# Optimization experiments

Hardware: AMD Instinct MI355X
Metric: run time of the kernel (lower is better)

## Reference

```python
import jax, jax.numpy as jnp
import numpy as np
import math

N, I, H, O = 2048, 16, 64, 64
CUTS, HEADS_DIM, GROUPS = 8, 8, 4
RADIUS = 1.0
EPS = 1e-5


def setup_inputs() -> dict:
    key = jax.random.key(0)
    ks = jax.random.split(key, 16)
    points = jax.random.normal(ks[0], (N, 3), dtype=jnp.float32) * 3.0
    nuv = jax.random.normal(ks[1], (N, 3, 3), dtype=jnp.float32)
    nuv = nuv / jnp.linalg.norm(nuv, axis=-1, keepdims=True)  # unit local basis rows [n,u,v]
    features = jax.random.normal(ks[2], (N, I), dtype=jnp.float32)
    # net_in
    W_in1 = jax.random.normal(ks[3], (H, I), dtype=jnp.float32) / math.sqrt(I)
    b_in1 = jnp.zeros((H,), jnp.float32)
    W_in2 = jax.random.normal(ks[4], (H, H), dtype=jnp.float32) / math.sqrt(H)
    b_in2 = jnp.zeros((H,), jnp.float32)
    gn_in_w = jnp.ones((H,), jnp.float32)
    gn_in_b = jnp.zeros((H,), jnp.float32)
    # radial conv MLP (matches the torch custom init)
    conv_w1 = jax.random.normal(ks[5], (CUTS, 3), dtype=jnp.float32)
    conv_b1 = jax.random.uniform(ks[6], (CUTS,), dtype=jnp.float32) * 0.8 * jnp.sqrt((conv_w1 ** 2).sum(-1))
    lim = 1.0 / math.sqrt(CUTS)
    conv_w2 = jax.random.uniform(ks[7], (H, CUTS), dtype=jnp.float32, minval=-lim, maxval=lim)
    conv_b2 = jax.random.normal(ks[8], (H,), dtype=jnp.float32) * 0.5 * jnp.sqrt((conv_w2 ** 2).sum(-1))
    # net_out
    W_out1 = jax.random.normal(ks[9], (O, H), dtype=jnp.float32) / math.sqrt(H)
    b_out1 = jnp.zeros((O,), jnp.float32)
    W_out2 = jax.random.normal(ks[10], (O, O), dtype=jnp.float32) / math.sqrt(O)
    b_out2 = jnp.zeros((O,), jnp.float32)
    gn_out_w = jnp.ones((O,), jnp.float32)
    gn_out_b = jnp.zeros((O,), jnp.float32)
    return dict(points=points, nuv=nuv, features=features,
                W_in1=W_in1, b_in1=b_in1, W_in2=W_in2, b_in2=b_in2,
                gn_in_w=gn_in_w, gn_in_b=gn_in_b,
                conv_w1=conv_w1, conv_b1=conv_b1, conv_w2=conv_w2, conv_b2=conv_b2,
                W_out1=W_out1, b_out1=b_out1, W_out2=W_out2, b_out2=b_out2,
                gn_out_w=gn_out_w, gn_out_b=gn_out_b)


def group_norm(x, w, b):
    # x: [N, C]; torch GroupNorm(4, C) on [1, C, N]: stats over (channels-in-group, N)
    n, c = x.shape
    xg = x.T.reshape(GROUPS, (c // GROUPS) * n)
    mean = xg.mean(axis=1, keepdims=True)
    var = xg.var(axis=1, keepdims=True)
    xg = (xg - mean) / jnp.sqrt(var + EPS)
    return xg.reshape(c, n).T * w + b


def reference(points, nuv, features,
              W_in1, b_in1, W_in2, b_in2, gn_in_w, gn_in_b,
              conv_w1, conv_b1, conv_w2, conv_b2,
              W_out1, b_out1, W_out2, b_out2, gn_out_w, gn_out_b):
    lrelu = lambda x: jax.nn.leaky_relu(x, 0.2)
    # net_in + GroupNorm
    f = lrelu(features @ W_in1.T + b_in1)
    f = lrelu(f @ W_in2.T + b_in2)
    f = group_norm(f, gn_in_w, gn_in_b)  # [N, H]
    # pseudo-geodesic window
    p = points / (math.sqrt(2.0) * RADIUS)
    diff = p[None, :, :] - p[:, None, :]          # x_j - x_i  [N, N, 3]
    normals = nuv[:, 0, :]
    ndot = normals @ normals.T                     # n_i . n_j  [N, N]
    d2 = jnp.sum(diff ** 2, axis=-1) * (2.0 - ndot) ** 2
    window = jnp.exp(-d2)                          # [N, N]
    # local-basis projection P_ij = nuv_i @ (x_j - x_i)
    P = jnp.einsum('iab,ijb->ija', nuv, diff)      # [N, N, 3]
    # first conv layer shared across heads
    h = jax.nn.relu(jnp.einsum('ijb,cb->ijc', P, conv_w1) + conv_b1)  # [N, N, CUTS]
    n_heads = H // HEADS_DIM
    outs = []
    for hd in range(n_heads):
        s = hd * HEADS_DIM
        e = s + HEADS_DIM
        X = jax.nn.relu(jnp.einsum('ijc,dc->ijd', h, conv_w2[s:e]) + conv_b2[s:e])  # [N, N, hd]
        outs.append(jnp.einsum('ij,ijd,jd->id', window, X, f[:, s:e]))
    f = jnp.concatenate(outs, axis=1)              # [N, H]
    # net_out + GroupNorm
    f = lrelu(f @ W_out1.T + b_out1)
    f = lrelu(f @ W_out2.T + b_out2)
    f = group_norm(f, gn_out_w, gn_out_b)          # [N, O]
    return f
```

## Files before the change

### kernel.cpp

```cpp
#include <hip/hip_runtime.h>
#include <math.h>
#include <stdint.h>

#define N_PTS 2048
#define I_DIM 16
#define H_DIM 64
#define O_DIM 64
#define NCUTS 8
#define NGROUPS 4
#define GN_EPS 1e-5f
#define GN_TOT 32768.0f

typedef __attribute__((ext_vector_type(8))) short short8;
typedef __attribute__((ext_vector_type(4))) float f32x4;
typedef __attribute__((ext_vector_type(4))) uint32_t u32x4;

__device__ inline uint32_t cvt_pk_bf16(float lo, float hi) {
    uint32_t r;
    asm("v_cvt_pk_bf16_f32 %0, %1, %2" : "=v"(r) : "v"(lo), "v"(hi));
    return r;
}

__device__ inline short8 frag_of(uint32_t a, uint32_t b, uint32_t c, uint32_t d) {
    u32x4 t; t.x = a; t.y = b; t.z = c; t.w = d;
    return __builtin_bit_cast(short8, t);
}

__device__ inline float bf16hi_to_f(uint32_t w) {
    return __builtin_bit_cast(float, w & 0xFFFF0000u);
}
__device__ inline float bf16lo_to_f(uint32_t w) {
    return __builtin_bit_cast(float, w << 16);
}

__global__ __launch_bounds__(256) void k_front(
    const float* __restrict__ points, const float* __restrict__ nuv,
    const float* __restrict__ features, const float* __restrict__ W1,
    const float* __restrict__ b1, const float* __restrict__ W2,
    const float* __restrict__ b2, float* __restrict__ out,
    float* __restrict__ pjp, float* __restrict__ stats)
{
    __shared__ float f0s[4][H_DIM];
    __shared__ float sred[16], qred[16];
    const float SC = 0.70710678118654752f;
    int tid = threadIdx.x;
    int pl = tid >> 6, h = tid & 63;
    int n = blockIdx.x * 4 + pl;

    if (h < 3)            pjp[n * 8 + h]     = points[n * 3 + h] * SC;
    else if (h == 3)      pjp[n * 8 + 3]     = 0.f;
    else if (h < 7)       pjp[n * 8 + h]     = nuv[n * 9 + (h - 4)];
    else if (h == 7)      pjp[n * 8 + 7]     = 0.f;

    const float* fr = features + n * I_DIM;
    float s = b1[h];
    #pragma unroll
    for (int i = 0; i < I_DIM; ++i) s = fmaf(fr[i], W1[h * I_DIM + i], s);
    s = s > 0.f ? s : 0.2f * s;
    f0s[pl][h] = s;
    __syncthreads();
    float t = b2[h];
    #pragma unroll
    for (int k = 0; k < H_DIM; ++k) t = fmaf(f0s[pl][k], W2[h * H_DIM + k], t);
    t = t > 0.f ? t : 0.2f * t;
    out[n * H_DIM + h] = t;

    float ss = t, qq = t * t;
    #pragma unroll
    for (int off = 8; off >= 1; off >>= 1) {
        ss += __shfl_xor(ss, off);
        qq += __shfl_xor(qq, off);
    }
    int grp = pl * 4 + (h >> 4);
    if ((h & 15) == 0) { sred[grp] = ss; qred[grp] = qq; }
    __syncthreads();
    if (tid < 4) {
        float S = sred[tid] + sred[4 + tid] + sred[8 + tid] + sred[12 + tid];
        float Q = qred[tid] + qred[4 + tid] + qred[8 + tid] + qred[12 + tid];
        atomicAdd(&stats[tid], S);
        atomicAdd(&stats[4 + tid], Q);
    }
}

__global__ __launch_bounds__(256) void k_apply1(
    const float* __restrict__ x, const float* __restrict__ stats,
    const float* __restrict__ w, const float* __restrict__ b,
    uint32_t* __restrict__ fbh)
{
    int idx2 = blockIdx.x * 256 + threadIdx.x;
    int e = idx2 * 2;
    int ch = e & 63;
    int g = ch >> 4;
    float m = stats[g] / GN_TOT;
    float var = stats[4 + g] / GN_TOT - m * m;
    float r = rsqrtf(var + GN_EPS);
    float v0 = (x[e]     - m) * r * w[ch]     + b[ch];
    float v1 = (x[e + 1] - m) * r * w[ch + 1] + b[ch + 1];
    fbh[idx2] = cvt_pk_bf16(v0, v1);
}

__global__ __launch_bounds__(256, 4) void k_conv_mfma(
    const float* __restrict__ pjp, const float* __restrict__ nuv,
    const float* __restrict__ cw1, const float* __restrict__ cb1,
    const float* __restrict__ cw2, const float* __restrict__ cb2,
    const uint32_t* __restrict__ fbh, float* __restrict__ out)
{
    __shared__ float red[4][H_DIM];
    int i   = blockIdx.x;
    int tid = threadIdx.x;
    int lane = tid & 63, wv = tid >> 6;
    int l15 = lane & 15, lg = lane >> 4;

    uint32_t one_b = cvt_pk_bf16(1.f, 0.f);
    uint32_t idx_b = cvt_pk_bf16((float)l15, 0.f);
    short8 pIdx = frag_of(lg == 0 ? idx_b : 0u, 0u, 0u, 0u);
    short8 pOne = frag_of(lg == 0 ? one_b : 0u, 0u, 0u, 0u);
    f32x4 Dc = __builtin_amdgcn_mfma_f32_16x16x32_bf16(
        pIdx, pOne, (f32x4){0.f, 0.f, 0.f, 0.f}, 0, 0, 0);
    f32x4 Dj = __builtin_amdgcn_mfma_f32_16x16x32_bf16(
        pOne, pIdx, (f32x4){0.f, 0.f, 0.f, 0.f}, 0, 0, 0);
    int cc[4];
    #pragma unroll
    for (int r = 0; r < 4; ++r) cc[r] = (int)(Dc[r] + 0.5f);
    int cc0 = cc[0];
    int jj0 = (int)(Dj[0] + 0.5f);
    int cc0q = cc0 >> 2;

    float pix = pjp[i * 8 + 0];
    float piy = pjp[i * 8 + 1];
    float piz = pjp[i * 8 + 2];
    float nv[9];
    #pragma unroll
    for (int a = 0; a < 9; ++a) nv[a] = nuv[i * 9 + a];
    float w1c[NCUTS][3], bb1[NCUTS];
    #pragma unroll
    for (int c = 0; c < NCUTS; ++c) {
        w1c[c][0] = cw1[c * 3 + 0];
        w1c[c][1] = cw1[c * 3 + 1];
        w1c[c][2] = cw1[c * 3 + 2];
        bb1[c]    = cb1[c];
    }

    short8 Af[4];
    #pragma unroll
    for (int m = 0; m < 4; ++m) {
        int ch = m * 16 + l15;
        uint32_t a0 = 0, a1 = 0, a2 = 0, a3 = 0;
        if (lg == 0) {
            a0 = cvt_pk_bf16(cw2[ch * 8 + 0], cw2[ch * 8 + 1]);
            a1 = cvt_pk_bf16(cw2[ch * 8 + 2], cw2[ch * 8 + 3]);
            a2 = cvt_pk_bf16(cw2[ch * 8 + 4], cw2[ch * 8 + 5]);
            a3 = cvt_pk_bf16(cw2[ch * 8 + 6], cw2[ch * 8 + 7]);
        } else if (lg == 1) {
            a0 = cvt_pk_bf16(cb2[ch], 0.f);
        }
        Af[m] = frag_of(a0, a1, a2, a3);
    }

    float acc[4][4];
    #pragma unroll
    for (int m = 0; m < 4; ++m)
        #pragma unroll
        for (int r = 0; r < 4; ++r) acc[m][r] = 0.f;

    const uint2* fh = (const uint2*)fbh;

    #pragma unroll 1
    for (int jt = wv; jt < N_PTS / 64; jt += 4) {
        int j = jt * 64 + lane;
        f32x4 pa = ((const f32x4*)pjp)[j * 2 + 0];
        f32x4 pb = ((const f32x4*)pjp)[j * 2 + 1];
        float dx = pa.x - pix;
        float dy = pa.y - piy;
        float dz = pa.z - piz;
        float nd = nv[0] * pb.x + nv[1] * pb.y + nv[2] * pb.z;
        float tt = 2.f - nd;
        float d2 = (dx * dx + dy * dy + dz * dz) * tt * tt;
        float win = __expf(-d2);
        float P0 = nv[0] * dx + nv[1] * dy + nv[2] * dz;
        float P1 = nv[3] * dx + nv[4] * dy + nv[5] * dz;
        float P2 = nv[6] * dx + nv[7] * dy + nv[8] * dz;
        float hp[NCUTS];
        #pragma unroll
        for (int c = 0; c < NCUTS; ++c) {
            float v = fmaf(P0, w1c[c][0], fmaf(P1, w1c[c][1], fmaf(P2, w1c[c][2], bb1[c])));
            v = v > 0.f ? v : 0.f;
            hp[c] = win * v;
        }
        uint32_t hw0 = cvt_pk_bf16(hp[0], hp[1]);
        uint32_t hw1 = cvt_pk_bf16(hp[2], hp[3]);
        uint32_t hw2 = cvt_pk_bf16(hp[4], hp[5]);
        uint32_t hw3 = cvt_pk_bf16(hp[6], hp[7]);
        uint32_t ww  = cvt_pk_bf16(win, 0.f);

        #pragma unroll
        for (int n = 0; n < 4; ++n) {
            int src = n * 16 + l15;
            uint32_t s0 = (uint32_t)__shfl((int)hw0, src);
            uint32_t s1 = (uint32_t)__shfl((int)hw1, src);
            uint32_t s2 = (uint32_t)__shfl((int)hw2, src);
            uint32_t s3 = (uint32_t)__shfl((int)hw3, src);
            uint32_t sw = (uint32_t)__shfl((int)ww , src);
            short8 Bf = frag_of(
                (lg == 0) ? s0 : ((lg == 1) ? sw : 0u),
                (lg == 0) ? s1 : 0u,
                (lg == 0) ? s2 : 0u,
                (lg == 0) ? s3 : 0u);
            int e2 = ((jt * 64 + n * 16 + jj0) << 4) + cc0q;
            #pragma unroll
            for (int m = 0; m < 4; ++m) {
                uint2 u = fh[e2 + m * 4];
                f32x4 C = __builtin_amdgcn_mfma_f32_16x16x32_bf16(
                    Af[m], Bf, (f32x4){0.f, 0.f, 0.f, 0.f}, 0, 0, 0);
                float f0 = bf16lo_to_f(u.x);
                float f1 = bf16hi_to_f(u.x);
                float f2 = bf16lo_to_f(u.y);
                float f3 = bf16hi_to_f(u.y);
                float x0 = C[0] > 0.f ? C[0] : 0.f;
                float x1 = C[1] > 0.f ? C[1] : 0.f;
                float x2 = C[2] > 0.f ? C[2] : 0.f;
                float x3 = C[3] > 0.f ? C[3] : 0.f;
                acc[m][0] = fmaf(x0, f0, acc[m][0]);
                acc[m][1] = fmaf(x1, f1, acc[m][1]);
                acc[m][2] = fmaf(x2, f2, acc[m][2]);
                acc[m][3] = fmaf(x3, f3, acc[m][3]);
            }
        }
    }

    #pragma unroll
    for (int m = 0; m < 4; ++m)
        #pragma unroll
        for (int r = 0; r < 4; ++r) {
            float v = acc[m][r];
            v += __shfl_xor(v, 1);
            v += __shfl_xor(v, 2);
            v += __shfl_xor(v, 4);
            v += __shfl_xor(v, 8);
            acc[m][r] = v;
        }

    if (l15 == 0) {
        #pragma unroll
        for (int m = 0; m < 4; ++m)
            #pragma unroll
            for (int r = 0; r < 4; ++r)
                red[wv][m * 16 + cc[r]] = acc[m][r];
    }
    __syncthreads();
    if (tid < H_DIM) {
        out[i * H_DIM + tid] = red[0][tid] + red[1][tid] + red[2][tid] + red[3][tid];
    }
}

__global__ __launch_bounds__(256) void k_back(
    const float* __restrict__ fin, const float* __restrict__ W1,
    const float* __restrict__ b1, const float* __restrict__ W2,
    const float* __restrict__ b2, float* __restrict__ out,
    float* __restrict__ stats)
{
    __shared__ float t1s[4][O_DIM];
    __shared__ float sred[16], qred[16];
    int tid = threadIdx.x;
    int pl = tid >> 6, o = tid & 63;
    int n = blockIdx.x * 4 + pl;
    const float* fr = fin + n * H_DIM;
    float s = b1[o];
    #pragma unroll
    for (int k = 0; k < H_DIM; ++k) s = fmaf(fr[k], W1[o * H_DIM + k], s);
    s = s > 0.f ? s : 0.2f * s;
    t1s[pl][o] = s;
    __syncthreads();
    float t = b2[o];
    #pragma unroll
    for (int k = 0; k < O_DIM; ++k) t = fmaf(t1s[pl][k], W2[o * O_DIM + k], t);
    t = t > 0.f ? t : 0.2f * t;
    out[n * O_DIM + o] = t;

    float ss = t, qq = t * t;
    #pragma unroll
    for (int off = 8; off >= 1; off >>= 1) {
        ss += __shfl_xor(ss, off);
        qq += __shfl_xor(qq, off);
    }
    int grp = pl * 4 + (o >> 4);
    if ((o & 15) == 0) { sred[grp] = ss; qred[grp] = qq; }
    __syncthreads();
    if (tid < 4) {
        float S = sred[tid] + sred[4 + tid] + sred[8 + tid] + sred[12 + tid];
        float Q = qred[tid] + qred[4 + tid] + qred[8 + tid] + qred[12 + tid];
        atomicAdd(&stats[tid], S);
        atomicAdd(&stats[4 + tid], Q);
    }
}

__global__ __launch_bounds__(256) void k_apply2(
    float* __restrict__ x, const float* __restrict__ stats,
    const float* __restrict__ w, const float* __restrict__ b)
{
    for (int idx = blockIdx.x * 256 + threadIdx.x; idx < N_PTS * O_DIM;
         idx += gridDim.x * 256) {
        int ch = idx & 63;
        int g = ch >> 4;
        float m = stats[g] / GN_TOT;
        float var = stats[4 + g] / GN_TOT - m * m;
        float r = rsqrtf(var + GN_EPS);
        x[idx] = (x[idx] - m) * r * w[ch] + b[ch];
    }
}

extern "C" void kernel_launch(void* const* d_in, const int* in_sizes, int n_in,
                              void* d_out, int out_size, void* d_ws, size_t ws_size,
                              hipStream_t stream)
{
    const float* points   = (const float*)d_in[0];
    const float* nuv      = (const float*)d_in[1];
    const float* features = (const float*)d_in[2];
    const float* W_in1    = (const float*)d_in[3];
    const float* b_in1    = (const float*)d_in[4];
    const float* W_in2    = (const float*)d_in[5];
    const float* b_in2    = (const float*)d_in[6];
    const float* gn_in_w  = (const float*)d_in[7];
    const float* gn_in_b  = (const float*)d_in[8];
    const float* cw1      = (const float*)d_in[9];
    const float* cb1      = (const float*)d_in[10];
    const float* cw2      = (const float*)d_in[11];
    const float* cb2      = (const float*)d_in[12];
    const float* W_out1   = (const float*)d_in[13];
    const float* b_out1   = (const float*)d_in[14];
    const float* W_out2   = (const float*)d_in[15];
    const float* b_out2   = (const float*)d_in[16];
    const float* gn_out_w = (const float*)d_in[17];
    const float* gn_out_b = (const float*)d_in[18];

    float*    bufA  = (float*)d_ws;
    float*    pjp   = bufA + N_PTS * H_DIM;
    float*    stats = pjp + N_PTS * 8;
    uint32_t* fbh   = (uint32_t*)(stats + 16);
    float*    outp  = (float*)d_out;

    hipMemsetAsync(stats, 0, 16 * sizeof(float), stream);
    k_front    <<<N_PTS / 4, 256, 0, stream>>>(points, nuv, features,
                                               W_in1, b_in1, W_in2, b_in2,
                                               bufA, pjp, stats);
    k_apply1   <<<N_PTS * H_DIM / 512, 256, 0, stream>>>(bufA, stats,
                                               gn_in_w, gn_in_b, fbh);
    k_conv_mfma<<<N_PTS, 256, 0, stream>>>(pjp, nuv, cw1, cb1, cw2, cb2,
                                               fbh, bufA);
    k_back     <<<N_PTS / 4, 256, 0, stream>>>(bufA, W_out1, b_out1,
                                               W_out2, b_out2, outp, stats + 8);
    k_apply2   <<<256, 256, 0, stream>>>(outp, stats + 8, gn_out_w, gn_out_b);
}
```

Baseline: 259.2 us.

## Switch conv to 32x32x16 MFMA and replace GroupNorm atomics with per-block partials

The pairwise conv kernel moves from 16x16x32 to 32x32x16 bf16 MFMA tiles. Each wave now builds two B fragments with a single xor-32 shuffle instead of 20 indexed shuffles per j-tile, and issues four larger MFMAs in place of sixteen small ones. The GroupNorm statistics no longer use global atomics plus a memset. Each block writes its partial sums and every apply block re-reduces all partials, which adds redundant reduction work in each apply block. The second apply kernel also gets a one-element-pair-per-thread grid with float2 access.

```diff
diff --git a/kernel.cpp b/kernel.cpp
--- a/kernel.cpp
+++ b/kernel.cpp
@@ -11,9 +11,10 @@
 #define GN_EPS 1e-5f
 #define GN_TOT 32768.0f
 
-typedef __attribute__((ext_vector_type(8))) short short8;
-typedef __attribute__((ext_vector_type(4))) float f32x4;
-typedef __attribute__((ext_vector_type(4))) uint32_t u32x4;
+typedef __attribute__((ext_vector_type(8)))  short    short8;
+typedef __attribute__((ext_vector_type(4)))  float    f32x4;
+typedef __attribute__((ext_vector_type(16))) float    f32x16;
+typedef __attribute__((ext_vector_type(4)))  uint32_t u32x4;
 
 __device__ inline uint32_t cvt_pk_bf16(float lo, float hi) {
     uint32_t r;
@@ -38,7 +39,7 @@
     const float* __restrict__ features, const float* __restrict__ W1,
     const float* __restrict__ b1, const float* __restrict__ W2,
     const float* __restrict__ b2, float* __restrict__ out,
-    float* __restrict__ pjp, float* __restrict__ stats)
+    float* __restrict__ pjp, float* __restrict__ part)
 {
     __shared__ float f0s[4][H_DIM];
     __shared__ float sred[16], qred[16];
@@ -47,10 +48,10 @@
     int pl = tid >> 6, h = tid & 63;
     int n = blockIdx.x * 4 + pl;
 
-    if (h < 3)            pjp[n * 8 + h]     = points[n * 3 + h] * SC;
-    else if (h == 3)      pjp[n * 8 + 3]     = 0.f;
-    else if (h < 7)       pjp[n * 8 + h]     = nuv[n * 9 + (h - 4)];
-    else if (h == 7)      pjp[n * 8 + 7]     = 0.f;
+    if (h < 3)            pjp[n * 8 + h] = points[n * 3 + h] * SC;
+    else if (h == 3)      pjp[n * 8 + 3] = 0.f;
+    else if (h < 7)       pjp[n * 8 + h] = nuv[n * 9 + (h - 4)];
+    else if (h == 7)      pjp[n * 8 + 7] = 0.f;
 
     const float* fr = features + n * I_DIM;
     float s = b1[h];
@@ -77,22 +78,44 @@
     if (tid < 4) {
         float S = sred[tid] + sred[4 + tid] + sred[8 + tid] + sred[12 + tid];
         float Q = qred[tid] + qred[4 + tid] + qred[8 + tid] + qred[12 + tid];
-        atomicAdd(&stats[tid], S);
-        atomicAdd(&stats[4 + tid], Q);
+        part[blockIdx.x * 8 + tid]     = S;
+        part[blockIdx.x * 8 + 4 + tid] = Q;
     }
 }
 
 __global__ __launch_bounds__(256) void k_apply1(
-    const float* __restrict__ x, const float* __restrict__ stats,
+    const float* __restrict__ x, const float* __restrict__ part,
     const float* __restrict__ w, const float* __restrict__ b,
     uint32_t* __restrict__ fbh)
 {
-    int idx2 = blockIdx.x * 256 + threadIdx.x;
+    __shared__ float s8[4][8];
+    int tid = threadIdx.x;
+    const f32x4* p4 = (const f32x4*)part;
+    f32x4 sa = p4[tid * 4 + 0], qa = p4[tid * 4 + 1];
+    f32x4 sb = p4[tid * 4 + 2], qb = p4[tid * 4 + 3];
+    float sv0 = sa.x + sb.x, sv1 = sa.y + sb.y, sv2 = sa.z + sb.z, sv3 = sa.w + sb.w;
+    float qv0 = qa.x + qb.x, qv1 = qa.y + qb.y, qv2 = qa.z + qb.z, qv3 = qa.w + qb.w;
+    #pragma unroll
+    for (int off = 1; off <= 32; off <<= 1) {
+        sv0 += __shfl_xor(sv0, off); sv1 += __shfl_xor(sv1, off);
+        sv2 += __shfl_xor(sv2, off); sv3 += __shfl_xor(sv3, off);
+        qv0 += __shfl_xor(qv0, off); qv1 += __shfl_xor(qv1, off);
+        qv2 += __shfl_xor(qv2, off); qv3 += __shfl_xor(qv3, off);
+    }
+    int lane = tid & 63, wvv = tid >> 6;
+    if (lane == 0) {
+        s8[wvv][0] = sv0; s8[wvv][1] = sv1; s8[wvv][2] = sv2; s8[wvv][3] = sv3;
+        s8[wvv][4] = qv0; s8[wvv][5] = qv1; s8[wvv][6] = qv2; s8[wvv][7] = qv3;
+    }
+    __syncthreads();
+    int idx2 = blockIdx.x * 256 + tid;
     int e = idx2 * 2;
     int ch = e & 63;
     int g = ch >> 4;
-    float m = stats[g] / GN_TOT;
-    float var = stats[4 + g] / GN_TOT - m * m;
+    float S = s8[0][g] + s8[1][g] + s8[2][g] + s8[3][g];
+    float Q = s8[0][4 + g] + s8[1][4 + g] + s8[2][4 + g] + s8[3][4 + g];
+    float m = S / GN_TOT;
+    float var = Q / GN_TOT - m * m;
     float r = rsqrtf(var + GN_EPS);
     float v0 = (x[e]     - m) * r * w[ch]     + b[ch];
     float v1 = (x[e + 1] - m) * r * w[ch + 1] + b[ch + 1];
@@ -109,22 +132,21 @@
     int i   = blockIdx.x;
     int tid = threadIdx.x;
     int lane = tid & 63, wv = tid >> 6;
-    int l15 = lane & 15, lg = lane >> 4;
+    int l31 = lane & 31, lg2 = lane >> 5;
+
+    const f32x16 z16 = {0.f,0.f,0.f,0.f,0.f,0.f,0.f,0.f,
+                        0.f,0.f,0.f,0.f,0.f,0.f,0.f,0.f};
 
     uint32_t one_b = cvt_pk_bf16(1.f, 0.f);
-    uint32_t idx_b = cvt_pk_bf16((float)l15, 0.f);
-    short8 pIdx = frag_of(lg == 0 ? idx_b : 0u, 0u, 0u, 0u);
-    short8 pOne = frag_of(lg == 0 ? one_b : 0u, 0u, 0u, 0u);
-    f32x4 Dc = __builtin_amdgcn_mfma_f32_16x16x32_bf16(
-        pIdx, pOne, (f32x4){0.f, 0.f, 0.f, 0.f}, 0, 0, 0);
-    f32x4 Dj = __builtin_amdgcn_mfma_f32_16x16x32_bf16(
-        pOne, pIdx, (f32x4){0.f, 0.f, 0.f, 0.f}, 0, 0, 0);
-    int cc[4];
-    #pragma unroll
-    for (int r = 0; r < 4; ++r) cc[r] = (int)(Dc[r] + 0.5f);
-    int cc0 = cc[0];
+    uint32_t idx_b = cvt_pk_bf16((float)l31, 0.f);
+    short8 pIdx = frag_of(lg2 == 0 ? idx_b : 0u, 0u, 0u, 0u);
+    short8 pOne = frag_of(lg2 == 0 ? one_b : 0u, 0u, 0u, 0u);
+    f32x16 Dc = __builtin_amdgcn_mfma_f32_32x32x16_bf16(pIdx, pOne, z16, 0, 0, 0);
+    f32x16 Dj = __builtin_amdgcn_mfma_f32_32x32x16_bf16(pOne, pIdx, z16, 0, 0, 0);
+    int ccq[4];
+    #pragma unroll
+    for (int q = 0; q < 4; ++q) ccq[q] = ((int)(Dc[4 * q] + 0.5f)) >> 2;
     int jj0 = (int)(Dj[0] + 0.5f);
-    int cc0q = cc0 >> 2;
 
     float pix = pjp[i * 8 + 0];
     float piy = pjp[i * 8 + 1];
@@ -141,27 +163,27 @@
         bb1[c]    = cb1[c];
     }
 
-    short8 Af[4];
-    #pragma unroll
-    for (int m = 0; m < 4; ++m) {
-        int ch = m * 16 + l15;
+    short8 Af[2];
+    #pragma unroll
+    for (int m = 0; m < 2; ++m) {
+        int ch = m * 32 + l31;
         uint32_t a0 = 0, a1 = 0, a2 = 0, a3 = 0;
-        if (lg == 0) {
+        if (lg2 == 0) {
             a0 = cvt_pk_bf16(cw2[ch * 8 + 0], cw2[ch * 8 + 1]);
             a1 = cvt_pk_bf16(cw2[ch * 8 + 2], cw2[ch * 8 + 3]);
             a2 = cvt_pk_bf16(cw2[ch * 8 + 4], cw2[ch * 8 + 5]);
             a3 = cvt_pk_bf16(cw2[ch * 8 + 6], cw2[ch * 8 + 7]);
-        } else if (lg == 1) {
+        } else {
             a0 = cvt_pk_bf16(cb2[ch], 0.f);
         }
         Af[m] = frag_of(a0, a1, a2, a3);
     }
 
-    float acc[4][4];
-    #pragma unroll
-    for (int m = 0; m < 4; ++m)
+    float acc[2][16];
+    #pragma unroll
+    for (int m = 0; m < 2; ++m)
         #pragma unroll
-        for (int r = 0; r < 4; ++r) acc[m][r] = 0.f;
+        for (int r = 0; r < 16; ++r) acc[m][r] = 0.f;
 
     const uint2* fh = (const uint2*)fbh;
 
@@ -193,59 +215,68 @@
         uint32_t hw3 = cvt_pk_bf16(hp[6], hp[7]);
         uint32_t ww  = cvt_pk_bf16(win, 0.f);
 
+        uint32_t wsw = (uint32_t)__shfl_xor((int)ww , 32);
+        uint32_t h0s = (uint32_t)__shfl_xor((int)hw0, 32);
+        uint32_t h1s = (uint32_t)__shfl_xor((int)hw1, 32);
+        uint32_t h2s = (uint32_t)__shfl_xor((int)hw2, 32);
+        uint32_t h3s = (uint32_t)__shfl_xor((int)hw3, 32);
+
+        short8 B0 = frag_of(lg2 == 0 ? hw0 : wsw,
+                            lg2 == 0 ? hw1 : 0u,
+                            lg2 == 0 ? hw2 : 0u,
+                            lg2 == 0 ? hw3 : 0u);
+        short8 B1 = frag_of(lg2 == 0 ? h0s : ww,
+                            lg2 == 0 ? h1s : 0u,
+                            lg2 == 0 ? h2s : 0u,
+                            lg2 == 0 ? h3s : 0u);
+
         #pragma unroll
-        for (int n = 0; n < 4; ++n) {
-            int src = n * 16 + l15;
-            uint32_t s0 = (uint32_t)__shfl((int)hw0, src);
-            uint32_t s1 = (uint32_t)__shfl((int)hw1, src);
-            uint32_t s2 = (uint32_t)__shfl((int)hw2, src);
-            uint32_t s3 = (uint32_t)__shfl((int)hw3, src);
-            uint32_t sw = (uint32_t)__shfl((int)ww , src);
-            short8 Bf = frag_of(
-                (lg == 0) ? s0 : ((lg == 1) ? sw : 0u),
-                (lg == 0) ? s1 : 0u,
-                (lg == 0) ? s2 : 0u,
-                (lg == 0) ? s3 : 0u);
-            int e2 = ((jt * 64 + n * 16 + jj0) << 4) + cc0q;
+        for (int ns = 0; ns < 2; ++ns) {
+            short8 Bf = ns ? B1 : B0;
+            int rowb = (jt * 64 + ns * 32 + jj0) * 16;
             #pragma unroll
-            for (int m = 0; m < 4; ++m) {
-                uint2 u = fh[e2 + m * 4];
-                f32x4 C = __builtin_amdgcn_mfma_f32_16x16x32_bf16(
-                    Af[m], Bf, (f32x4){0.f, 0.f, 0.f, 0.f}, 0, 0, 0);
-                float f0 = bf16lo_to_f(u.x);
-                float f1 = bf16hi_to_f(u.x);
-                float f2 = bf16lo_to_f(u.y);
-                float f3 = bf16hi_to_f(u.y);
-                float x0 = C[0] > 0.f ? C[0] : 0.f;
-                float x1 = C[1] > 0.f ? C[1] : 0.f;
-                float x2 = C[2] > 0.f ? C[2] : 0.f;
-                float x3 = C[3] > 0.f ? C[3] : 0.f;
-                acc[m][0] = fmaf(x0, f0, acc[m][0]);
-                acc[m][1] = fmaf(x1, f1, acc[m][1]);
-                acc[m][2] = fmaf(x2, f2, acc[m][2]);
-                acc[m][3] = fmaf(x3, f3, acc[m][3]);
+            for (int m = 0; m < 2; ++m) {
+                f32x16 C = __builtin_amdgcn_mfma_f32_32x32x16_bf16(
+                    Af[m], Bf, z16, 0, 0, 0);
+                #pragma unroll
+                for (int q = 0; q < 4; ++q) {
+                    uint2 u = fh[rowb + m * 8 + ccq[q]];
+                    float f0 = bf16lo_to_f(u.x);
+                    float f1 = bf16hi_to_f(u.x);
+                    float f2 = bf16lo_to_f(u.y);
+                    float f3 = bf16hi_to_f(u.y);
+                    float x0 = fmaxf(C[4 * q + 0], 0.f);
+                    float x1 = fmaxf(C[4 * q + 1], 0.f);
+                    float x2 = fmaxf(C[4 * q + 2], 0.f);
+                    float x3 = fmaxf(C[4 * q + 3], 0.f);
+                    acc[m][4 * q + 0] = fmaf(x0, f0, acc[m][4 * q + 0]);
+                    acc[m][4 * q + 1] = fmaf(x1, f1, acc[m][4 * q + 1]);
+                    acc[m][4 * q + 2] = fmaf(x2, f2, acc[m][4 * q + 2]);
+                    acc[m][4 * q + 3] = fmaf(x3, f3, acc[m][4 * q + 3]);
+                }
             }
         }
     }
 
     #pragma unroll
-    for (int m = 0; m < 4; ++m)
+    for (int m = 0; m < 2; ++m)
         #pragma unroll
-        for (int r = 0; r < 4; ++r) {
+        for (int r = 0; r < 16; ++r) {
             float v = acc[m][r];
             v += __shfl_xor(v, 1);
             v += __shfl_xor(v, 2);
             v += __shfl_xor(v, 4);
             v += __shfl_xor(v, 8);
+            v += __shfl_xor(v, 16);
             acc[m][r] = v;
         }
 
-    if (l15 == 0) {
+    if (l31 == 0) {
         #pragma unroll
-        for (int m = 0; m < 4; ++m)
+        for (int m = 0; m < 2; ++m)
             #pragma unroll
-            for (int r = 0; r < 4; ++r)
-                red[wv][m * 16 + cc[r]] = acc[m][r];
+            for (int r = 0; r < 16; ++r)
+                red[wv][m * 32 + (ccq[r >> 2] << 2) + (r & 3)] = acc[m][r];
     }
     __syncthreads();
     if (tid < H_DIM) {
@@ -257,7 +288,7 @@
     const float* __restrict__ fin, const float* __restrict__ W1,
     const float* __restrict__ b1, const float* __restrict__ W2,
     const float* __restrict__ b2, float* __restrict__ out,
-    float* __restrict__ stats)
+    float* __restrict__ part)
 {
     __shared__ float t1s[4][O_DIM];
     __shared__ float sred[16], qred[16];
@@ -289,24 +320,48 @@
     if (tid < 4) {
         float S = sred[tid] + sred[4 + tid] + sred[8 + tid] + sred[12 + tid];
         float Q = qred[tid] + qred[4 + tid] + qred[8 + tid] + qred[12 + tid];
-        atomicAdd(&stats[tid], S);
-        atomicAdd(&stats[4 + tid], Q);
+        part[blockIdx.x * 8 + tid]     = S;
+        part[blockIdx.x * 8 + 4 + tid] = Q;
     }
 }
 
 __global__ __launch_bounds__(256) void k_apply2(
-    float* __restrict__ x, const float* __restrict__ stats,
+    float* __restrict__ x, const float* __restrict__ part,
     const float* __restrict__ w, const float* __restrict__ b)
 {
-    for (int idx = blockIdx.x * 256 + threadIdx.x; idx < N_PTS * O_DIM;
-         idx += gridDim.x * 256) {
-        int ch = idx & 63;
-        int g = ch >> 4;
-        float m = stats[g] / GN_TOT;
-        float var = stats[4 + g] / GN_TOT - m * m;
-        float r = rsqrtf(var + GN_EPS);
-        x[idx] = (x[idx] - m) * r * w[ch] + b[ch];
-    }
+    __shared__ float s8[4][8];
+    int tid = threadIdx.x;
+    const f32x4* p4 = (const f32x4*)part;
+    f32x4 sa = p4[tid * 4 + 0], qa = p4[tid * 4 + 1];
+    f32x4 sb = p4[tid * 4 + 2], qb = p4[tid * 4 + 3];
+    float sv0 = sa.x + sb.x, sv1 = sa.y + sb.y, sv2 = sa.z + sb.z, sv3 = sa.w + sb.w;
+    float qv0 = qa.x + qb.x, qv1 = qa.y + qb.y, qv2 = qa.z + qb.z, qv3 = qa.w + qb.w;
+    #pragma unroll
+    for (int off = 1; off <= 32; off <<= 1) {
+        sv0 += __shfl_xor(sv0, off); sv1 += __shfl_xor(sv1, off);
+        sv2 += __shfl_xor(sv2, off); sv3 += __shfl_xor(sv3, off);
+        qv0 += __shfl_xor(qv0, off); qv1 += __shfl_xor(qv1, off);
+        qv2 += __shfl_xor(qv2, off); qv3 += __shfl_xor(qv3, off);
+    }
+    int lane = tid & 63, wvv = tid >> 6;
+    if (lane == 0) {
+        s8[wvv][0] = sv0; s8[wvv][1] = sv1; s8[wvv][2] = sv2; s8[wvv][3] = sv3;
+        s8[wvv][4] = qv0; s8[wvv][5] = qv1; s8[wvv][6] = qv2; s8[wvv][7] = qv3;
+    }
+    __syncthreads();
+    int idx2 = blockIdx.x * 256 + tid;
+    int e = idx2 * 2;
+    int ch = e & 63;
+    int g = ch >> 4;
+    float S = s8[0][g] + s8[1][g] + s8[2][g] + s8[3][g];
+    float Q = s8[0][4 + g] + s8[1][4 + g] + s8[2][4 + g] + s8[3][4 + g];
+    float m = S / GN_TOT;
+    float var = Q / GN_TOT - m * m;
+    float r = rsqrtf(var + GN_EPS);
+    float2 v = ((const float2*)x)[idx2];
+    float v0 = (v.x - m) * r * w[ch]     + b[ch];
+    float v1 = (v.y - m) * r * w[ch + 1] + b[ch + 1];
+    ((float2*)x)[idx2] = make_float2(v0, v1);
 }
 
 extern "C" void kernel_launch(void* const* d_in, const int* in_sizes, int n_in,
@@ -335,19 +390,20 @@
 
     float*    bufA  = (float*)d_ws;
     float*    pjp   = bufA + N_PTS * H_DIM;
-    float*    stats = pjp + N_PTS * 8;
-    uint32_t* fbh   = (uint32_t*)(stats + 16);
+    uint32_t* fbh   = (uint32_t*)(pjp + N_PTS * 8);
+    float*    part1 = (float*)(fbh + N_PTS * 32);
+    float*    part2 = part1 + 512 * 8;
     float*    outp  = (float*)d_out;
 
-    hipMemsetAsync(stats, 0, 16 * sizeof(float), stream);
     k_front    <<<N_PTS / 4, 256, 0, stream>>>(points, nuv, features,
                                                W_in1, b_in1, W_in2, b_in2,
-                                               bufA, pjp, stats);
-    k_apply1   <<<N_PTS * H_DIM / 512, 256, 0, stream>>>(bufA, stats,
+                                               bufA, pjp, part1);
+    k_apply1   <<<N_PTS * H_DIM / 512, 256, 0, stream>>>(bufA, part1,
                                                gn_in_w, gn_in_b, fbh);
     k_conv_mfma<<<N_PTS, 256, 0, stream>>>(pjp, nuv, cw1, cb1, cw2, cb2,
                                                fbh, bufA);
     k_back     <<<N_PTS / 4, 256, 0, stream>>>(bufA, W_out1, b_out1,
-                                               W_out2, b_out2, outp, stats + 8);
-    k_apply2   <<<256, 256, 0, stream>>>(outp, stats + 8, gn_out_w, gn_out_b);
-}
+                                               W_out2, b_out2, outp, part2);
+    k_apply2   <<<N_PTS * O_DIM / 512, 256, 0, stream>>>(outp, part2,
+                                               gn_out_w, gn_out_b);
+}
```

After: 295.9 us. 14.1% more time.
